# Kernel tuning notes

Hardware: AMD Instinct MI355X
Metric: run time of the kernel (lower is better)

The kernel has to match this reference:

```python
import jax, jax.numpy as jnp
import numpy as np

B, S, H = 32, 512, 768
V = 8192
W_MAX = 256  # max words per sample after merging subwords


def setup_inputs() -> dict:
    key = jax.random.key(0)
    k1, k2, k3 = jax.random.split(key, 3)
    bert_encodings = jax.random.normal(k1, (B, S, H), dtype=jnp.float32)
    # per-token word index, sorted per row -> contiguous ragged segments
    segment_ids = jnp.sort(jax.random.randint(k2, (B, S), 0, W_MAX, dtype=jnp.int32), axis=1)
    W = jax.random.normal(k3, (H, V), dtype=jnp.float32) * 0.02
    b = jnp.zeros((V,), dtype=jnp.float32)
    return {
        "bert_encodings": bert_encodings,
        "segment_ids": segment_ids,
        "W": W,
        "b": b,
        "num_words": W_MAX,
    }


def reference(bert_encodings, segment_ids, W, b, num_words):
    Bb, Ss, Hh = bert_encodings.shape
    # Flatten batch: give each sample its own block of segment ids so one
    # segment_sum handles the whole batch (fused segment-reduce).
    flat_ids = (segment_ids + jnp.arange(Bb, dtype=segment_ids.dtype)[:, None] * num_words).reshape(-1)
    flat_enc = bert_encodings.reshape(-1, Hh)
    sums = jax.ops.segment_sum(flat_enc, flat_ids, num_segments=Bb * num_words)  # [B*W, H]
    counts = jax.ops.segment_sum(jnp.ones((Bb * Ss,), dtype=flat_enc.dtype), flat_ids,
                                 num_segments=Bb * num_words)  # [B*W]
    # mean per word; words with no subwords are zero-padded (like pad_sequence)
    denom = jnp.where(counts > 0, counts, 1.0)[:, None]
    merged = jnp.where(counts[:, None] > 0, sums / denom, 0.0).reshape(Bb, num_words, Hh)
    logits = jnp.einsum("bwh,hv->bwv", merged, W) + b  # [B, W_MAX, V]
    return logits
```

## Files before the change

### kernel.cpp

```cpp
#include <hip/hip_runtime.h>
#include <cstdint>
#include <cstddef>

typedef unsigned short ushort_t;
typedef __bf16 bf16x8 __attribute__((ext_vector_type(8)));
typedef float f32x4 __attribute__((ext_vector_type(4)));

__device__ __forceinline__ ushort_t f2bf(float x) {
    union { float f; uint32_t u; } v; v.f = x;
    return (ushort_t)((v.u + 0x7FFFu + ((v.u >> 16) & 1u)) >> 16);
}

__device__ __forceinline__ void gld_lds16(const void* g, void* l) {
    __builtin_amdgcn_global_load_lds(
        (const __attribute__((address_space(1))) uint32_t*)g,
        (__attribute__((address_space(3))) uint32_t*)l,
        16, 0, 0);
}

__global__ __launch_bounds__(256) void transpose_convert(
    const float* __restrict__ Wm, ushort_t* __restrict__ Wt, int H, int V)
{
    __shared__ ushort_t tile[64][65];
    const int v0 = blockIdx.x * 64;
    const int k0 = blockIdx.y * 64;
    const int tx = threadIdx.x & 63;
    const int ty = threadIdx.x >> 6;

    #pragma unroll
    for (int i = ty; i < 64; i += 4)
        tile[i][tx] = f2bf(Wm[(size_t)(k0 + i) * V + v0 + tx]);
    __syncthreads();
    #pragma unroll
    for (int i = ty; i < 64; i += 4)
        Wt[(size_t)(v0 + i) * H + k0 + tx] = tile[tx][i];
}

__global__ __launch_bounds__(256) void seg_mean(
    const float* __restrict__ enc,
    const int*   __restrict__ seg,
    ushort_t*    __restrict__ merged,
    int S, int H, int W)
{
    const int bw = blockIdx.x;
    const int b  = bw / W;
    const int w  = bw - b * W;
    const int* srow = seg + (size_t)b * S;

    int l = 0, r = S;
    while (l < r) { int m = (l + r) >> 1; if (srow[m] < w) l = m + 1; else r = m; }
    const int lo = l;
    r = S;
    while (l < r) { int m = (l + r) >> 1; if (srow[m] < w + 1) l = m + 1; else r = m; }
    const int hi = l;

    const int cnt = hi - lo;
    const float scale = (cnt > 0) ? (1.0f / (float)cnt) : 0.0f;
    const float* erow = enc + (size_t)b * S * H;
    ushort_t* orow = merged + (size_t)bw * H;

    for (int h = threadIdx.x; h < H; h += 256) {
        float s = 0.0f;
        for (int t = lo; t < hi; ++t) s += erow[(size_t)t * H + h];
        orow[h] = f2bf(s * scale);
    }
}

__global__ __launch_bounds__(256) void gemm_bt(
    const ushort_t* __restrict__ A,
    const ushort_t* __restrict__ Bt,
    const float*    __restrict__ bias,
    float*          __restrict__ C,
    int M, int N, int K)
{
    __shared__ ushort_t As[128 * 32];
    __shared__ ushort_t Bs[128 * 32];

    const int tid  = threadIdx.x;
    const int wave = tid >> 6;
    const int lane = tid & 63;
    const int wm   = wave >> 1;
    const int wn   = wave & 1;
    const int r15  = lane & 15;
    const int quad = lane >> 4;

    const int m0 = blockIdx.y * 128;
    const int n0 = blockIdx.x * 128;

    const int srow = tid >> 2;
    const int scol = (tid & 3) * 8;

    const ushort_t* Ag = A  + (size_t)(m0 + srow) * K + scol;
    const ushort_t* Bg = Bt + (size_t)(n0 + srow) * K + scol;
    ushort_t* AsW = As + wave * 512;
    ushort_t* BsW = Bs + wave * 512;

    f32x4 acc[4][4] = {};

    const ushort_t* a_lds = As + (wm * 64 + r15) * 32 + quad * 8;
    const ushort_t* b_lds = Bs + (wn * 64 + r15) * 32 + quad * 8;

    for (int kt = 0; kt < K; kt += 32) {
        gld_lds16(Ag + kt,                   AsW);
        gld_lds16(Ag + (size_t)64 * K + kt,  AsW + 2048);
        gld_lds16(Bg + kt,                   BsW);
        gld_lds16(Bg + (size_t)64 * K + kt,  BsW + 2048);
        __syncthreads();

        bf16x8 af[4], bf[4];
        #pragma unroll
        for (int i = 0; i < 4; ++i) {
            af[i] = *(const bf16x8*)(a_lds + i * 16 * 32);
            bf[i] = *(const bf16x8*)(b_lds + i * 16 * 32);
        }
        #pragma unroll
        for (int i = 0; i < 4; ++i)
            #pragma unroll
            for (int j = 0; j < 4; ++j)
                acc[i][j] = __builtin_amdgcn_mfma_f32_16x16x32_bf16(
                                af[i], bf[j], acc[i][j], 0, 0, 0);
        __syncthreads();
    }

    const int crow = m0 + wm * 64 + quad * 4;
    const int ccol = n0 + wn * 64 + r15;
    #pragma unroll
    for (int j = 0; j < 4; ++j) {
        const float bv = bias[ccol + j * 16];
        #pragma unroll
        for (int i = 0; i < 4; ++i) {
            float* cp = C + (size_t)(crow + i * 16) * N + (ccol + j * 16);
            #pragma unroll
            for (int r = 0; r < 4; ++r)
                cp[(size_t)r * N] = acc[i][j][r] + bv;
        }
    }
}

extern "C" void kernel_launch(void* const* d_in, const int* in_sizes, int n_in,
                              void* d_out, int out_size, void* d_ws, size_t ws_size,
                              hipStream_t stream) {
    const float* enc  = (const float*)d_in[0];
    const int*   seg  = (const int*)d_in[1];
    const float* Wm   = (const float*)d_in[2];
    const float* bias = (const float*)d_in[3];

    const int B = 32, S = 512, H = 768, V = 8192, WMAX = 256;
    const int M = B * WMAX;

    ushort_t* Wt     = (ushort_t*)d_ws;
    ushort_t* merged = Wt + (size_t)V * H;
    float*    out    = (float*)d_out;

    hipLaunchKernelGGL(transpose_convert, dim3(V / 64, H / 64), dim3(256), 0, stream,
                       Wm, Wt, H, V);
    hipLaunchKernelGGL(seg_mean, dim3(M), dim3(256), 0, stream,
                       enc, seg, merged, S, H, WMAX);
    hipLaunchKernelGGL(gemm_bt, dim3(V / 128, M / 128), dim3(256), 0, stream,
                       merged, Wt, bias, out, M, V, H);
}
```

Measured before the change: 458.4 us.

## Vectorize transpose and segment-mean, process K=64 per GEMM iteration

The weight transpose now reads float4 and writes 16-byte bf16 vectors through a padded LDS tile. The segment mean gives one wave to each word and uses float4 loads. The GEMM loads two 32-wide K slices per barrier pair, which halves the number of synchronisations and doubles the shared memory used. The aim is fewer memory transactions in the preprocessing kernels and less barrier overhead in the GEMM. The new transpose LDS writes may hit bank conflicts, and seg_mean now hardcodes W=256 through shifts.

```diff
diff --git a/kernel.cpp b/kernel.cpp
--- a/kernel.cpp
+++ b/kernel.cpp
@@ -5,6 +5,9 @@
 typedef unsigned short ushort_t;
 typedef __bf16 bf16x8 __attribute__((ext_vector_type(8)));
 typedef float f32x4 __attribute__((ext_vector_type(4)));
+typedef float f32x4v __attribute__((ext_vector_type(4)));
+typedef unsigned short u16x4 __attribute__((ext_vector_type(4)));
+typedef unsigned short u16x8 __attribute__((ext_vector_type(8)));
 
 __device__ __forceinline__ ushort_t f2bf(float x) {
     union { float f; uint32_t u; } v; v.f = x;
@@ -21,19 +24,30 @@
 __global__ __launch_bounds__(256) void transpose_convert(
     const float* __restrict__ Wm, ushort_t* __restrict__ Wt, int H, int V)
 {
-    __shared__ ushort_t tile[64][65];
+    __shared__ ushort_t tile[64][72];
     const int v0 = blockIdx.x * 64;
     const int k0 = blockIdx.y * 64;
-    const int tx = threadIdx.x & 63;
-    const int ty = threadIdx.x >> 6;
+    const int tid = threadIdx.x;
 
     #pragma unroll
-    for (int i = ty; i < 64; i += 4)
-        tile[i][tx] = f2bf(Wm[(size_t)(k0 + i) * V + v0 + tx]);
+    for (int p = 0; p < 4; ++p) {
+        const int krow = p * 16 + (tid >> 4);
+        const int vcol = (tid & 15) * 4;
+        const f32x4v w = *(const f32x4v*)&Wm[(size_t)(k0 + krow) * V + v0 + vcol];
+        tile[vcol + 0][krow] = f2bf(w.x);
+        tile[vcol + 1][krow] = f2bf(w.y);
+        tile[vcol + 2][krow] = f2bf(w.z);
+        tile[vcol + 3][krow] = f2bf(w.w);
+    }
     __syncthreads();
     #pragma unroll
-    for (int i = ty; i < 64; i += 4)
-        Wt[(size_t)(v0 + i) * H + k0 + tx] = tile[tx][i];
+    for (int p = 0; p < 2; ++p) {
+        const int idx = p * 256 + tid;
+        const int v = idx >> 3;
+        const int c = (idx & 7) * 8;
+        const u16x8 val = *(const u16x8*)&tile[v][c];
+        *(u16x8*)&Wt[(size_t)(v0 + v) * H + k0 + c] = val;
+    }
 }
 
 __global__ __launch_bounds__(256) void seg_mean(
@@ -42,9 +56,11 @@
     ushort_t*    __restrict__ merged,
     int S, int H, int W)
 {
-    const int bw = blockIdx.x;
-    const int b  = bw / W;
-    const int w  = bw - b * W;
+    const int wave = threadIdx.x >> 6;
+    const int lane = threadIdx.x & 63;
+    const int bw = blockIdx.x * 4 + wave;
+    const int b  = bw >> 8;
+    const int w  = bw & 255;
     const int* srow = seg + (size_t)b * S;
 
     int l = 0, r = S;
@@ -59,10 +75,18 @@
     const float* erow = enc + (size_t)b * S * H;
     ushort_t* orow = merged + (size_t)bw * H;
 
-    for (int h = threadIdx.x; h < H; h += 256) {
-        float s = 0.0f;
-        for (int t = lo; t < hi; ++t) s += erow[(size_t)t * H + h];
-        orow[h] = f2bf(s * scale);
+    #pragma unroll
+    for (int c = 0; c < 3; ++c) {
+        const int col = c * 256 + lane * 4;
+        f32x4v s = {0.f, 0.f, 0.f, 0.f};
+        for (int t = lo; t < hi; ++t) {
+            const f32x4v v = *(const f32x4v*)&erow[(size_t)t * H + col];
+            s.x += v.x; s.y += v.y; s.z += v.z; s.w += v.w;
+        }
+        u16x4 o;
+        o.x = f2bf(s.x * scale); o.y = f2bf(s.y * scale);
+        o.z = f2bf(s.z * scale); o.w = f2bf(s.w * scale);
+        *(u16x4*)&orow[col] = o;
     }
 }
 
@@ -73,8 +97,8 @@
     float*          __restrict__ C,
     int M, int N, int K)
 {
-    __shared__ ushort_t As[128 * 32];
-    __shared__ ushort_t Bs[128 * 32];
+    __shared__ ushort_t As[2][128 * 32];
+    __shared__ ushort_t Bs[2][128 * 32];
 
     const int tid  = threadIdx.x;
     const int wave = tid >> 6;
@@ -92,33 +116,39 @@
 
     const ushort_t* Ag = A  + (size_t)(m0 + srow) * K + scol;
     const ushort_t* Bg = Bt + (size_t)(n0 + srow) * K + scol;
-    ushort_t* AsW = As + wave * 512;
-    ushort_t* BsW = Bs + wave * 512;
+    const int wofs = wave * 512;
 
     f32x4 acc[4][4] = {};
 
-    const ushort_t* a_lds = As + (wm * 64 + r15) * 32 + quad * 8;
-    const ushort_t* b_lds = Bs + (wn * 64 + r15) * 32 + quad * 8;
+    const int a_fo = (wm * 64 + r15) * 32 + quad * 8;
+    const int b_fo = (wn * 64 + r15) * 32 + quad * 8;
 
-    for (int kt = 0; kt < K; kt += 32) {
-        gld_lds16(Ag + kt,                   AsW);
-        gld_lds16(Ag + (size_t)64 * K + kt,  AsW + 2048);
-        gld_lds16(Bg + kt,                   BsW);
-        gld_lds16(Bg + (size_t)64 * K + kt,  BsW + 2048);
+    for (int kt = 0; kt < K; kt += 64) {
+        gld_lds16(Ag + kt,                        &As[0][wofs]);
+        gld_lds16(Ag + (size_t)64 * K + kt,       &As[0][wofs + 2048]);
+        gld_lds16(Bg + kt,                        &Bs[0][wofs]);
+        gld_lds16(Bg + (size_t)64 * K + kt,       &Bs[0][wofs + 2048]);
+        gld_lds16(Ag + kt + 32,                   &As[1][wofs]);
+        gld_lds16(Ag + (size_t)64 * K + kt + 32,  &As[1][wofs + 2048]);
+        gld_lds16(Bg + kt + 32,                   &Bs[1][wofs]);
+        gld_lds16(Bg + (size_t)64 * K + kt + 32,  &Bs[1][wofs + 2048]);
         __syncthreads();
 
-        bf16x8 af[4], bf[4];
         #pragma unroll
-        for (int i = 0; i < 4; ++i) {
-            af[i] = *(const bf16x8*)(a_lds + i * 16 * 32);
-            bf[i] = *(const bf16x8*)(b_lds + i * 16 * 32);
+        for (int h = 0; h < 2; ++h) {
+            bf16x8 af[4], bf[4];
+            #pragma unroll
+            for (int i = 0; i < 4; ++i) {
+                af[i] = *(const bf16x8*)(&As[h][a_fo + i * 16 * 32]);
+                bf[i] = *(const bf16x8*)(&Bs[h][b_fo + i * 16 * 32]);
+            }
+            #pragma unroll
+            for (int i = 0; i < 4; ++i)
+                #pragma unroll
+                for (int j = 0; j < 4; ++j)
+                    acc[i][j] = __builtin_amdgcn_mfma_f32_16x16x32_bf16(
+                                    af[i], bf[j], acc[i][j], 0, 0, 0);
         }
-        #pragma unroll
-        for (int i = 0; i < 4; ++i)
-            #pragma unroll
-            for (int j = 0; j < 4; ++j)
-                acc[i][j] = __builtin_amdgcn_mfma_f32_16x16x32_bf16(
-                                af[i], bf[j], acc[i][j], 0, 0, 0);
         __syncthreads();
     }
 
@@ -154,7 +184,7 @@
 
     hipLaunchKernelGGL(transpose_convert, dim3(V / 64, H / 64), dim3(256), 0, stream,
                        Wm, Wt, H, V);
-    hipLaunchKernelGGL(seg_mean, dim3(M), dim3(256), 0, stream,
+    hipLaunchKernelGGL(seg_mean, dim3(M / 4), dim3(256), 0, stream,
                        enc, seg, merged, S, H, WMAX);
     hipLaunchKernelGGL(gemm_bt, dim3(V / 128, M / 128), dim3(256), 0, stream,
                        merged, Wt, bias, out, M, V, H);
```

Result: no change. 449.8 us (-1.9%).
